# Kernel optimization log

Hardware: AMD Instinct MI355X
Metric: run time of the kernel (lower is better)

The kernel has to match this reference:

```python
import jax, jax.numpy as jnp
import numpy as np

N_X = 20000      # bessel x-grid
N_ELL = 48       # sparse tabulated multipoles
N_K = 1024       # k quadrature points
N_TAU = 600      # conformal-time samples
K_PIVOT = 0.05


def fast_interp(x, xmin, xmax, ytab):
    """Uniform-grid linear interpolation (tools.fast_interp). ytab: [Nx]."""
    n = ytab.shape[0]
    pos = jnp.clip((x - xmin) / (xmax - xmin) * (n - 1), 0.0, n - 1.0)
    i0 = jnp.clip(jnp.floor(pos).astype(jnp.int32), 0, n - 2)
    w = pos - i0
    return ytab[i0] * (1.0 - w) + ytab[i0 + 1] * w


def setup_inputs() -> dict:
    key = jax.random.key(0)
    ks = jax.random.split(key, 8)
    k = jnp.logspace(-4.0, 0.0, N_K, dtype=jnp.float32)           # Mpc^-1
    tau = jnp.linspace(50.0, 14000.0, N_TAU, dtype=jnp.float32)    # Mpc
    tau0 = jnp.asarray(14100.0, dtype=jnp.float32)
    bessel_x_tab = jnp.linspace(0.0, 15000.0, N_X, dtype=jnp.float32)
    mk = lambda kk, sh, s: (s * jax.random.normal(kk, sh, dtype=jnp.float32))
    return {
        "k": k,
        "tau": tau,
        "tau0": tau0,
        "S0": mk(ks[0], (N_K, N_TAU), 1e-2),
        "S1": mk(ks[1], (N_K, N_TAU), 1e-2),
        "S2": mk(ks[2], (N_K, N_TAU), 1e-2),
        "SE": mk(ks[3], (N_K, N_TAU), 1e-2),
        "bessel_x_tab": bessel_x_tab,
        "phi0_tab": mk(ks[4], (N_X, N_ELL), 1e-1),
        "phi1_tab": mk(ks[5], (N_X, N_ELL), 1e-1),
        "phi2_tab": mk(ks[6], (N_X, N_ELL), 1e-1),
        "eps_tab": mk(ks[7], (N_X, N_ELL), 1e-1),
        "A_s": jnp.asarray(2.1e-9, dtype=jnp.float32),
        "n_s": jnp.asarray(0.965, dtype=jnp.float32),
    }


def reference(k, tau, tau0, S0, S1, S2, SE, bessel_x_tab,
              phi0_tab, phi1_tab, phi2_tab, eps_tab, A_s, n_s):
    xmin = bessel_x_tab[0]
    xmax = bessel_x_tab[-1]
    # radial argument x = k * (tau0 - tau): [K, T]
    x = k[:, None] * (tau0 - tau)[None, :]

    def one_ell(p0, p1, p2, pe):
        # lookup phi0/phi1/phi2/epsilon at every (k, tau), fuse with sources
        srcT = (S0 * fast_interp(x, xmin, xmax, p0)
                + S1 * fast_interp(x, xmin, xmax, p1)
                + S2 * fast_interp(x, xmin, xmax, p2))
        Tl = jnp.trapezoid(srcT, tau, axis=-1)                       # [K]
        El = jnp.trapezoid(SE * fast_interp(x, xmin, xmax, pe), tau, axis=-1)
        return Tl, El

    # vmap over the tabulated-ell axis (columns of the Bessel tables)
    Tl, El = jax.vmap(one_ell, in_axes=(1, 1, 1, 1))(
        phi0_tab, phi1_tab, phi2_tab, eps_tab)                       # [L, K]

    # primordial curvature spectrum P_R(k) = A_s (k/k_p)^(n_s-1) * 2 pi^2 / k^3
    P_R = A_s * (k / K_PIVOT) ** (n_s - 1.0) * (2.0 * jnp.pi ** 2 / k ** 3)
    w = k * k * P_R                                                   # [K]
    c = 2.0 / jnp.pi
    ClTT = c * jnp.trapezoid(w * Tl * Tl, k, axis=-1)                 # [L]
    ClEE = c * jnp.trapezoid(w * El * El, k, axis=-1)
    ClTE = c * jnp.trapezoid(w * Tl * El, k, axis=-1)
    return jnp.stack([ClTT, ClEE, ClTE], axis=0)                      # [3, L]
```

## Files before the change

kernel.cpp:

```cpp
#include <hip/hip_runtime.h>
#include <math.h>

#define N_X   20000
#define N_ELL 48
#define N_K   1024
#define N_TAU 600
#define SPLIT 4
#define CHUNK (N_TAU / SPLIT)

__device__ __forceinline__ unsigned int bf16_rne(float f) {
    unsigned int u = __float_as_uint(f);
    return (u + 0x7FFFu + ((u >> 16) & 1u)) >> 16;
}
__device__ __forceinline__ float bf16_lo(unsigned int w) { return __uint_as_float(w << 16); }
__device__ __forceinline__ float bf16_hi(unsigned int w) { return __uint_as_float(w & 0xFFFF0000u); }

__global__ __launch_bounds__(256) void repack_kernel(
    const float* __restrict__ p0, const float* __restrict__ p1,
    const float* __restrict__ p2, const float* __restrict__ pe,
    uint2* __restrict__ P)
{
    const int total = N_X * N_ELL;
    for (int idx = blockIdx.x * blockDim.x + threadIdx.x; idx < total;
         idx += gridDim.x * blockDim.x) {
        uint2 v;
        v.x = bf16_rne(p0[idx]) | (bf16_rne(p1[idx]) << 16);
        v.y = bf16_rne(p2[idx]) | (bf16_rne(pe[idx]) << 16);
        P[idx] = v;
    }
}

__global__ __launch_bounds__(256) void tl_el_packed(
    const float* __restrict__ k, const float* __restrict__ tau,
    const float* __restrict__ tau0p,
    const float* __restrict__ S0, const float* __restrict__ S1,
    const float* __restrict__ S2, const float* __restrict__ SE,
    const float* __restrict__ bx, const uint2* __restrict__ P,
    float* __restrict__ Tlp, float* __restrict__ Elp)
{
    const int bid  = blockIdx.x;
    const int part = bid & (SPLIT - 1);
    const int kidx = (N_K - 1) - (bid >> 2);
    const int t0   = part * CHUNK;
    const int tid  = threadIdx.x;
    const int wave = tid >> 6;
    const int lane = tid & 63;
    const int ell  = (lane < N_ELL) ? lane : (N_ELL - 1);

    __shared__ unsigned int off_s[CHUNK];
    __shared__ float        w_s[CHUNK];
    __shared__ float4       S4_s[CHUNK];
    __shared__ float        redT[4][N_ELL];
    __shared__ float        redE[4][N_ELL];

    const float kk    = k[kidx];
    const float tau0  = tau0p[0];
    const float xmin  = bx[0];
    const float xmax  = bx[N_X - 1];
    const float scale = (float)(N_X - 1) / (xmax - xmin);

    if (tid < CHUNK) {
        int t = t0 + tid;
        float tt = tau[t];
        float tp = (t > 0)         ? tau[t - 1] : tt;
        float tn = (t < N_TAU - 1) ? tau[t + 1] : tt;
        float wt = 0.5f * (tn - tp);
        float x   = kk * (tau0 - tt);
        float pos = (x - xmin) * scale;
        pos = fminf(fmaxf(pos, 0.0f), (float)(N_X - 1));
        int i0 = (int)pos;
        if (i0 > N_X - 2) i0 = N_X - 2;
        off_s[tid] = (unsigned int)i0 * (N_ELL * 8u);
        w_s[tid]   = pos - (float)i0;
        size_t sb = (size_t)kidx * N_TAU + t;
        float4 s;
        s.x = wt * S0[sb];
        s.y = wt * S1[sb];
        s.z = wt * S2[sb];
        s.w = wt * SE[sb];
        S4_s[tid] = s;
    }
    __syncthreads();

    float accT = 0.0f, accE = 0.0f;
    const char* Pbase = (const char*)P;
    const unsigned int ell8 = (unsigned int)ell * 8u;

    #pragma unroll 4
    for (int i = wave; i < CHUNK; i += 4) {
        unsigned int voff = off_s[i] + ell8;
        float  w = w_s[i];
        float4 s = S4_s[i];

        uint2 ra = *(const uint2*)(Pbase + voff);
        uint2 rb = *(const uint2*)(Pbase + voff + N_ELL*8);

        float a0 = bf16_lo(ra.x), a1 = bf16_hi(ra.x);
        float a2 = bf16_lo(ra.y), ae = bf16_hi(ra.y);
        float b0 = bf16_lo(rb.x), b1 = bf16_hi(rb.x);
        float b2 = bf16_lo(rb.y), be = bf16_hi(rb.y);

        float v0 = fmaf(w, b0 - a0, a0);
        float v1 = fmaf(w, b1 - a1, a1);
        float v2 = fmaf(w, b2 - a2, a2);
        float ve = fmaf(w, be - ae, ae);

        float tacc = s.x * v0;
        tacc = fmaf(s.y, v1, tacc);
        tacc = fmaf(s.z, v2, tacc);
        accT += tacc;
        accE = fmaf(s.w, ve, accE);
    }

    if (lane < N_ELL) { redT[wave][lane] = accT; redE[wave][lane] = accE; }
    __syncthreads();
    if (tid < N_ELL) {
        float sT = (redT[0][tid] + redT[1][tid]) + (redT[2][tid] + redT[3][tid]);
        float sE = (redE[0][tid] + redE[1][tid]) + (redE[2][tid] + redE[3][tid]);
        Tlp[((size_t)part * N_ELL + tid) * N_K + kidx] = sT;
        Elp[((size_t)part * N_ELL + tid) * N_K + kidx] = sE;
    }
}

__global__ __launch_bounds__(256) void tl_el_kernel(
    const float* __restrict__ k, const float* __restrict__ tau,
    const float* __restrict__ tau0p,
    const float* __restrict__ S0, const float* __restrict__ S1,
    const float* __restrict__ S2, const float* __restrict__ SE,
    const float* __restrict__ bx,
    const float* __restrict__ p0, const float* __restrict__ p1,
    const float* __restrict__ p2, const float* __restrict__ pe,
    float* __restrict__ Tl, float* __restrict__ El)
{
    const int kidx = blockIdx.x;
    const int tid  = threadIdx.x;
    const int wave = tid >> 6;
    const int lane = tid & 63;
    const int ell  = (lane < N_ELL) ? lane : (N_ELL - 1);

    const float kk    = k[kidx];
    const float tau0  = tau0p[0];
    const float xmin  = bx[0];
    const float xmax  = bx[N_X - 1];
    const float scale = (float)(N_X - 1) / (xmax - xmin);

    const float* Srow0 = S0 + (size_t)kidx * N_TAU;
    const float* Srow1 = S1 + (size_t)kidx * N_TAU;
    const float* Srow2 = S2 + (size_t)kidx * N_TAU;
    const float* SrowE = SE + (size_t)kidx * N_TAU;

    float accT = 0.0f, accE = 0.0f;

    for (int t = wave; t < N_TAU; t += 4) {
        float tt    = tau[t];
        float tprev = (t > 0)         ? tau[t - 1] : tt;
        float tnext = (t < N_TAU - 1) ? tau[t + 1] : tt;
        float wt    = 0.5f * (tnext - tprev);

        float x   = kk * (tau0 - tt);
        float pos = (x - xmin) * scale;
        pos = fminf(fmaxf(pos, 0.0f), (float)(N_X - 1));
        int i0 = (int)floorf(pos);
        if (i0 > N_X - 2) i0 = N_X - 2;
        float w = pos - (float)i0;

        int base = i0 * N_ELL + ell;
        float y00 = p0[base], y01 = p0[base + N_ELL];
        float y10 = p1[base], y11 = p1[base + N_ELL];
        float y20 = p2[base], y21 = p2[base + N_ELL];
        float ye0 = pe[base], ye1 = pe[base + N_ELL];

        float a0 = fmaf(w, y01 - y00, y00);
        float a1 = fmaf(w, y11 - y10, y10);
        float a2 = fmaf(w, y21 - y20, y20);
        float ae = fmaf(w, ye1 - ye0, ye0);

        float s0 = Srow0[t], s1 = Srow1[t], s2 = Srow2[t], se = SrowE[t];

        float srcT = s0 * a0 + s1 * a1 + s2 * a2;
        accT = fmaf(wt, srcT, accT);
        accE = fmaf(wt, se * ae, accE);
    }

    __shared__ float redT[4][N_ELL];
    __shared__ float redE[4][N_ELL];
    if (lane < N_ELL) { redT[wave][lane] = accT; redE[wave][lane] = accE; }
    __syncthreads();
    if (tid < N_ELL) {
        float sT = (redT[0][tid] + redT[1][tid]) + (redT[2][tid] + redT[3][tid]);
        float sE = (redE[0][tid] + redE[1][tid]) + (redE[2][tid] + redE[3][tid]);
        Tl[tid * N_K + kidx] = sT;
        El[tid * N_K + kidx] = sE;
    }
}

__global__ __launch_bounds__(256) void cl_kernel(
    const float* __restrict__ k,
    const float* __restrict__ Asp, const float* __restrict__ nsp,
    const float* __restrict__ Tlp, const float* __restrict__ Elp,
    int nparts, float* __restrict__ out)
{
    const int ell = blockIdx.x;
    const int tid = threadIdx.x;
    const float A_s = Asp[0];
    const float n_s = nsp[0];
    const float two_pi2 = 2.0f * (float)M_PI * (float)M_PI;

    float aTT = 0.0f, aEE = 0.0f, aTE = 0.0f;
    for (int i = tid; i < N_K; i += 256) {
        float kv    = k[i];
        float kprev = (i > 0)       ? k[i - 1] : kv;
        float knext = (i < N_K - 1) ? k[i + 1] : kv;
        float dkw   = 0.5f * (knext - kprev);
        float Pw = A_s * powf(kv / 0.05f, n_s - 1.0f) * two_pi2 / kv;
        float ww = dkw * Pw;
        float tl = 0.0f, el = 0.0f;
        for (int p = 0; p < nparts; ++p) {
            tl += Tlp[((size_t)p * N_ELL + ell) * N_K + i];
            el += Elp[((size_t)p * N_ELL + ell) * N_K + i];
        }
        aTT = fmaf(ww * tl, tl, aTT);
        aEE = fmaf(ww * el, el, aEE);
        aTE = fmaf(ww * tl, el, aTE);
    }

    for (int off = 32; off > 0; off >>= 1) {
        aTT += __shfl_down(aTT, off, 64);
        aEE += __shfl_down(aEE, off, 64);
        aTE += __shfl_down(aTE, off, 64);
    }
    __shared__ float red[3][4];
    const int wave = tid >> 6, lane = tid & 63;
    if (lane == 0) { red[0][wave] = aTT; red[1][wave] = aEE; red[2][wave] = aTE; }
    __syncthreads();
    if (tid == 0) {
        const float c = 2.0f / (float)M_PI;
        out[0 * N_ELL + ell] = c * ((red[0][0] + red[0][1]) + (red[0][2] + red[0][3]));
        out[1 * N_ELL + ell] = c * ((red[1][0] + red[1][1]) + (red[1][2] + red[1][3]));
        out[2 * N_ELL + ell] = c * ((red[2][0] + red[2][1]) + (red[2][2] + red[2][3]));
    }
}

extern "C" void kernel_launch(void* const* d_in, const int* in_sizes, int n_in,
                              void* d_out, int out_size, void* d_ws, size_t ws_size,
                              hipStream_t stream) {
    const float* k    = (const float*)d_in[0];
    const float* tau  = (const float*)d_in[1];
    const float* tau0 = (const float*)d_in[2];
    const float* S0   = (const float*)d_in[3];
    const float* S1   = (const float*)d_in[4];
    const float* S2   = (const float*)d_in[5];
    const float* SE   = (const float*)d_in[6];
    const float* bx   = (const float*)d_in[7];
    const float* p0   = (const float*)d_in[8];
    const float* p1   = (const float*)d_in[9];
    const float* p2   = (const float*)d_in[10];
    const float* pe   = (const float*)d_in[11];
    const float* A_s  = (const float*)d_in[12];
    const float* n_s  = (const float*)d_in[13];
    float* out = (float*)d_out;

    const size_t P_bytes    = (size_t)N_X * N_ELL * sizeof(uint2);
    const size_t part_bytes = (size_t)SPLIT * N_ELL * N_K * sizeof(float);

    if (ws_size >= P_bytes + 2 * part_bytes) {
        uint2* P   = (uint2*)d_ws;
        float* Tlp = (float*)((char*)d_ws + P_bytes);
        float* Elp = (float*)((char*)d_ws + P_bytes + part_bytes);

        repack_kernel<<<(N_X * N_ELL + 255) / 256, 256, 0, stream>>>(p0, p1, p2, pe, P);
        tl_el_packed<<<N_K * SPLIT, 256, 0, stream>>>(k, tau, tau0, S0, S1, S2, SE, bx,
                                                      P, Tlp, Elp);
        cl_kernel<<<N_ELL, 256, 0, stream>>>(k, A_s, n_s, Tlp, Elp, SPLIT, out);
    } else {
        float* Tl = (float*)d_ws;
        float* El = Tl + (size_t)N_ELL * N_K;
        tl_el_kernel<<<N_K, 256, 0, stream>>>(k, tau, tau0, S0, S1, S2, SE, bx,
                                              p0, p1, p2, pe, Tl, El);
        cl_kernel<<<N_ELL, 256, 0, stream>>>(k, A_s, n_s, Tl, El, 1, out);
    }
}
```

Measured before the change: 144.9 us.

## Pack neighbor table entries as fp16 pairs and interpolate with v_dot2

The repack now stores each table entry together with its next-x neighbor as fp16 pairs (16 bytes per ell per x), so the main loop issues one 16-byte load instead of two 8-byte loads. The interpolation weights are folded into fp16-packed source coefficients, which lets each term become a single v_dot2_f32_f16 instruction. This trades bf16 for fp16 storage, which has less range but more mantissa, doubles the size of the packed table, and quantizes the source×weight products to fp16, which could underflow given sources around 1e-2 and tau weights.

Result: faster. 134.4 us (median of 2 runs) (-7.2%).

```diff
diff --git a/kernel.cpp b/kernel.cpp
--- a/kernel.cpp
+++ b/kernel.cpp
@@ -8,24 +8,35 @@
 #define SPLIT 4
 #define CHUNK (N_TAU / SPLIT)
 
-__device__ __forceinline__ unsigned int bf16_rne(float f) {
-    unsigned int u = __float_as_uint(f);
-    return (u + 0x7FFFu + ((u >> 16) & 1u)) >> 16;
-}
-__device__ __forceinline__ float bf16_lo(unsigned int w) { return __uint_as_float(w << 16); }
-__device__ __forceinline__ float bf16_hi(unsigned int w) { return __uint_as_float(w & 0xFFFF0000u); }
+__device__ __forceinline__ unsigned int pack_half2(float lo, float hi) {
+    _Float16 l = (_Float16)lo, h = (_Float16)hi;
+    unsigned short lu = __builtin_bit_cast(unsigned short, l);
+    unsigned short hu = __builtin_bit_cast(unsigned short, h);
+    return (unsigned int)lu | ((unsigned int)hu << 16);
+}
+__device__ __forceinline__ float fdot2(unsigned int a, unsigned int b, float c) {
+    float d;
+    asm("v_dot2_f32_f16 %0, %1, %2, %3" : "=v"(d) : "v"(a), "v"(b), "v"(c));
+    return d;
+}
 
 __global__ __launch_bounds__(256) void repack_kernel(
     const float* __restrict__ p0, const float* __restrict__ p1,
     const float* __restrict__ p2, const float* __restrict__ pe,
-    uint2* __restrict__ P)
+    uint4* __restrict__ P)
 {
     const int total = N_X * N_ELL;
     for (int idx = blockIdx.x * blockDim.x + threadIdx.x; idx < total;
          idx += gridDim.x * blockDim.x) {
-        uint2 v;
-        v.x = bf16_rne(p0[idx]) | (bf16_rne(p1[idx]) << 16);
-        v.y = bf16_rne(p2[idx]) | (bf16_rne(pe[idx]) << 16);
+        int x = idx / N_ELL;
+        int e = idx - x * N_ELL;
+        int xn = (x < N_X - 1) ? x + 1 : x;
+        int a = x * N_ELL + e, b = xn * N_ELL + e;
+        uint4 v;
+        v.x = pack_half2(p0[a], p0[b]);
+        v.y = pack_half2(p1[a], p1[b]);
+        v.z = pack_half2(p2[a], p2[b]);
+        v.w = pack_half2(pe[a], pe[b]);
         P[idx] = v;
     }
 }
@@ -35,7 +46,7 @@
     const float* __restrict__ tau0p,
     const float* __restrict__ S0, const float* __restrict__ S1,
     const float* __restrict__ S2, const float* __restrict__ SE,
-    const float* __restrict__ bx, const uint2* __restrict__ P,
+    const float* __restrict__ bx, const uint4* __restrict__ P,
     float* __restrict__ Tlp, float* __restrict__ Elp)
 {
     const int bid  = blockIdx.x;
@@ -48,8 +59,7 @@
     const int ell  = (lane < N_ELL) ? lane : (N_ELL - 1);
 
     __shared__ unsigned int off_s[CHUNK];
-    __shared__ float        w_s[CHUNK];
-    __shared__ float4       S4_s[CHUNK];
+    __shared__ uint4        W2_s[CHUNK];
     __shared__ float        redT[4][N_ELL];
     __shared__ float        redE[4][N_ELL];
 
@@ -70,49 +80,38 @@
         pos = fminf(fmaxf(pos, 0.0f), (float)(N_X - 1));
         int i0 = (int)pos;
         if (i0 > N_X - 2) i0 = N_X - 2;
-        off_s[tid] = (unsigned int)i0 * (N_ELL * 8u);
-        w_s[tid]   = pos - (float)i0;
+        float w  = pos - (float)i0;
+        float om = 1.0f - w;
         size_t sb = (size_t)kidx * N_TAU + t;
-        float4 s;
-        s.x = wt * S0[sb];
-        s.y = wt * S1[sb];
-        s.z = wt * S2[sb];
-        s.w = wt * SE[sb];
-        S4_s[tid] = s;
-    }
-    __syncthreads();
-
-    float accT = 0.0f, accE = 0.0f;
-    const char* Pbase = (const char*)P;
-    const unsigned int ell8 = (unsigned int)ell * 8u;
+        float s0 = wt * S0[sb], s1 = wt * S1[sb];
+        float s2 = wt * S2[sb], se = wt * SE[sb];
+        uint4 w2;
+        w2.x = pack_half2(s0 * om, s0 * w);
+        w2.y = pack_half2(s1 * om, s1 * w);
+        w2.z = pack_half2(s2 * om, s2 * w);
+        w2.w = pack_half2(se * om, se * w);
+        W2_s[tid]  = w2;
+        off_s[tid] = (unsigned int)i0 * (N_ELL * 16u);
+    }
+    __syncthreads();
+
+    const char* Pb = (const char*)P;
+    const unsigned int elloff = (unsigned int)ell * 16u;
+    float aT0 = 0.0f, aT1 = 0.0f, aT2 = 0.0f, aE = 0.0f;
 
     #pragma unroll 4
     for (int i = wave; i < CHUNK; i += 4) {
-        unsigned int voff = off_s[i] + ell8;
-        float  w = w_s[i];
-        float4 s = S4_s[i];
-
-        uint2 ra = *(const uint2*)(Pbase + voff);
-        uint2 rb = *(const uint2*)(Pbase + voff + N_ELL*8);
-
-        float a0 = bf16_lo(ra.x), a1 = bf16_hi(ra.x);
-        float a2 = bf16_lo(ra.y), ae = bf16_hi(ra.y);
-        float b0 = bf16_lo(rb.x), b1 = bf16_hi(rb.x);
-        float b2 = bf16_lo(rb.y), be = bf16_hi(rb.y);
-
-        float v0 = fmaf(w, b0 - a0, a0);
-        float v1 = fmaf(w, b1 - a1, a1);
-        float v2 = fmaf(w, b2 - a2, a2);
-        float ve = fmaf(w, be - ae, ae);
-
-        float tacc = s.x * v0;
-        tacc = fmaf(s.y, v1, tacc);
-        tacc = fmaf(s.z, v2, tacc);
-        accT += tacc;
-        accE = fmaf(s.w, ve, accE);
-    }
-
-    if (lane < N_ELL) { redT[wave][lane] = accT; redE[wave][lane] = accE; }
+        unsigned int voff = off_s[i] + elloff;
+        uint4 pr = *(const uint4*)(Pb + voff);
+        uint4 w2 = W2_s[i];
+        aT0 = fdot2(pr.x, w2.x, aT0);
+        aT1 = fdot2(pr.y, w2.y, aT1);
+        aT2 = fdot2(pr.z, w2.z, aT2);
+        aE  = fdot2(pr.w, w2.w, aE);
+    }
+    float accT = (aT0 + aT1) + aT2;
+
+    if (lane < N_ELL) { redT[wave][lane] = accT; redE[wave][lane] = aE; }
     __syncthreads();
     if (tid < N_ELL) {
         float sT = (redT[0][tid] + redT[1][tid]) + (redT[2][tid] + redT[3][tid]);
@@ -260,11 +259,11 @@
     const float* n_s  = (const float*)d_in[13];
     float* out = (float*)d_out;
 
-    const size_t P_bytes    = (size_t)N_X * N_ELL * sizeof(uint2);
+    const size_t P_bytes    = (size_t)N_X * N_ELL * sizeof(uint4);
     const size_t part_bytes = (size_t)SPLIT * N_ELL * N_K * sizeof(float);
 
     if (ws_size >= P_bytes + 2 * part_bytes) {
-        uint2* P   = (uint2*)d_ws;
+        uint4* P   = (uint4*)d_ws;
         float* Tlp = (float*)((char*)d_ws + P_bytes);
         float* Elp = (float*)((char*)d_ws + P_bytes + part_bytes);
 
```
